# Kernel tuning notes

Hardware: AMD Instinct MI355X
Metric: run time of the kernel (lower is better)

Reference implementation:

```python
import jax, jax.numpy as jnp
import numpy as np

B, N, D, H, K = 16, 256, 64, 64, 2  # batch, nodes, d_in, d_hidden, top_k


def setup_inputs() -> dict:
    key = jax.random.key(0)
    k0, k1, k2 = jax.random.split(key, 3)
    O = jax.random.normal(k0, (B, N, D), dtype=jnp.float32)
    # PairwiseFeaturizer.proj: Linear(4*D, H) -> ReLU -> Linear(H, 1)
    W1 = jax.random.normal(k1, (4 * D, H), dtype=jnp.float32) / np.sqrt(4 * D).astype(np.float32)
    b1 = jnp.zeros((H,), dtype=jnp.float32)
    W2 = jax.random.normal(k2, (H, 1), dtype=jnp.float32) / np.sqrt(H).astype(np.float32)
    b2 = jnp.zeros((1,), dtype=jnp.float32)
    return {"O": O, "W1": W1, "b1": b1, "W2": W2, "b2": b2}


def reference(O, W1, b1, W2, b2):
    Bn, Nn, d = O.shape
    ii, jj = jnp.triu_indices(Nn, k=1)  # all undirected pairs i<j, M = N(N-1)/2
    Oi = O[:, ii, :]  # (B, M, d) gather
    Oj = O[:, jj, :]  # (B, M, d) gather
    feats = jnp.concatenate([Oi, Oj, jnp.abs(Oi - Oj), Oi * Oj], axis=-1)  # (B, M, 4d)
    h = jax.nn.relu(jnp.einsum('bmf,fh->bmh', feats, W1) + b1)
    Q = (jnp.einsum('bmh,ho->bmo', h, W2) + b2)[..., 0]  # (B, M)
    # greedy top-k selection mask (eps -> 0 limit of select_pairs)
    idx = jax.lax.top_k(Q, K)[1]  # (B, K)
    mask = jnp.zeros(Q.shape, dtype=bool).at[jnp.arange(Q.shape[0])[:, None], idx].set(True)
    return Q, mask
```

## Files before the change

kernel.cpp:

```cpp
#include <hip/hip_runtime.h>
#include <math.h>

#define Bn 16
#define Nn 256
#define Mm (Nn*(Nn-1)/2)
#define CHUNK 4080

typedef __attribute__((ext_vector_type(8))) short bf16x8;
typedef __attribute__((ext_vector_type(4))) short short4v;
typedef __attribute__((ext_vector_type(4))) float f32x4;

typedef union { bf16x8 v; short s[8]; __bf16 h[8]; } F8;
typedef union { short4v v; __bf16 h[4]; } F4;

#define MFMA(acc, a, b) \
  acc = __builtin_amdgcn_mfma_f32_16x16x32_bf16((a), (b), (acc), 0, 0, 0)

__device__ __forceinline__ void top2_update(float v, int m,
    float& v1, int& i1, float& v2, int& i2)
{
  bool c1 = (v > v1) || (v == v1 && m < i1);
  bool c2 = (v > v2) || (v == v2 && m < i2);
  float nv2 = c1 ? v1 : (c2 ? v : v2);
  int   ni2 = c1 ? i1 : (c2 ? m : i2);
  v1 = c1 ? v : v1;  i1 = c1 ? m : i1;
  v2 = nv2;          i2 = ni2;
}

__global__ __launch_bounds__(256) void prep_w1t(
    const float* __restrict__ W1, unsigned short* __restrict__ wtg)
{
  const int h = blockIdx.x;
  const int k = threadIdx.x;
  __bf16 b = (__bf16)W1[k * 64 + h];
  wtg[h * 256 + k] = *(unsigned short*)&b;
}

__global__ __launch_bounds__(256) void prep_ac(
    const float* __restrict__ O, const float* __restrict__ b1,
    const unsigned short* __restrict__ wtg,
    unsigned short* __restrict__ obg, float* __restrict__ Ag,
    unsigned short* __restrict__ Cgb)
{
  __shared__ __align__(16) unsigned short s_ob[64][72];
  const int t = threadIdx.x, l = t & 63, wv = t >> 6;
  const int lo = l & 15, g = l >> 4;
  const int b = blockIdx.x >> 2, rt = blockIdx.x & 3;
  const int r0 = rt * 64;
  const float* Ob = O + ((size_t)b * Nn + r0) * 64;

  #pragma unroll
  for (int p = 0; p < 4; ++p) {
    int v = t + p * 256;
    int r = v >> 4, c4 = (v & 15) * 4;
    float4 x = ((const float4*)Ob)[v];
    F4 pk; pk.h[0] = (__bf16)x.x; pk.h[1] = (__bf16)x.y;
           pk.h[2] = (__bf16)x.z; pk.h[3] = (__bf16)x.w;
    *(short4v*)&s_ob[r][c4] = pk.v;
    *(short4v*)&obg[((size_t)b * Nn + r0 + r) * 64 + c4] = pk.v;
  }
  __syncthreads();

  F8 aop[2];
  #pragma unroll
  for (int ks = 0; ks < 2; ++ks)
    aop[ks].v = *(const bf16x8*)&s_ob[wv * 16 + lo][ks * 32 + g * 8];

  #pragma unroll
  for (int half = 0; half < 2; ++half) {
    #pragma unroll
    for (int nf = 0; nf < 4; ++nf) {
      f32x4 ac = {0.f, 0.f, 0.f, 0.f};
      #pragma unroll
      for (int ks = 0; ks < 2; ++ks) {
        F8 bop; bop.v = *(const bf16x8*)&wtg[(nf * 16 + lo) * 256 + half * 64 + ks * 32 + g * 8];
        MFMA(ac, aop[ks].v, bop.v);
      }
      const int h = nf * 16 + lo;
      if (half == 0) {
        float bb = b1[h];
        #pragma unroll
        for (int r = 0; r < 4; ++r)
          Ag[((size_t)b * Nn + r0 + wv * 16 + g * 4 + r) * 64 + h] = ac[r] + bb;
      } else {
        #pragma unroll
        for (int r = 0; r < 4; ++r) {
          __bf16 cb = (__bf16)ac[r];
          Cgb[((size_t)b * Nn + r0 + wv * 16 + g * 4 + r) * 64 + h] = *(unsigned short*)&cb;
        }
      }
    }
  }
}

__global__ __launch_bounds__(256, 2) void pair_kernel(
    const unsigned short* __restrict__ obg,
    const float* __restrict__ Ag,
    const unsigned short* __restrict__ Cgb,
    const float* __restrict__ W2,
    const float* __restrict__ b2,
    const unsigned short* __restrict__ wtg,
    float* __restrict__ Q,
    float* __restrict__ cand)
{
  __shared__ __align__(16) unsigned short s_wt[64][136];
  __shared__ float s_w2[64];
  __shared__ float s_red[4][4];

  const int t  = threadIdx.x;
  const int l  = t & 63, wv = t >> 6;
  const int lo = l & 15, g = l >> 4;

  const int blk    = blockIdx.x;
  const int within = blk >> 3;
  const int batch  = (blk & 7) * 2 + within / 72;
  int tl           = within % 72;
  int a = 0;
  while (tl >= 8 - (a >> 1)) { tl -= 8 - (a >> 1); ++a; }
  const int c   = (a >> 1) + tl;
  const int ti0 = a * 16, tj0 = c * 32;
  const bool diag = (tj0 == ti0 * 2 && (a & 1) == 0) ? false : false;
  const bool dg = (c * 32 < ti0 + 16) || (c == 0 && a == 0) ? false : false; (void)dg;
  const bool isdiag = (tj0 < ti0 + 16);

  const size_t obase = (size_t)batch * Nn;
  const size_t qbase = (size_t)batch * Mm;

  {
    const int h = t >> 2, kq = (t & 3) * 32;
    #pragma unroll
    for (int q = 0; q < 4; ++q)
      *(bf16x8*)&s_wt[h][kq + q * 8] =
          *(const bf16x8*)&wtg[h * 256 + 128 + kq + q * 8];
    if (t < 64) s_w2[t] = W2[t];
  }
  __syncthreads();

  F8 bfr[4][4];
  #pragma unroll
  for (int ks = 0; ks < 4; ++ks)
    #pragma unroll
    for (int nf = 0; nf < 4; ++nf)
      bfr[ks][nf].v = *(const bf16x8*)&s_wt[nf * 16 + lo][ks * 32 + g * 8];

  F8 ojb[2][2];
  #pragma unroll
  for (int jh = 0; jh < 2; ++jh) {
    ojb[jh][0].v = *(const bf16x8*)&obg[(obase + tj0 + jh * 16 + lo) * 64 + g * 8];
    ojb[jh][1].v = *(const bf16x8*)&obg[(obase + tj0 + jh * 16 + lo) * 64 + 32 + g * 8];
  }
  F4 cinb[2][4];
  #pragma unroll
  for (int jh = 0; jh < 2; ++jh)
    #pragma unroll
    for (int nf = 0; nf < 4; ++nf)
      cinb[jh][nf].v = *(const short4v*)
          &Cgb[(obase + tj0 + jh * 16 + lo) * 64 + nf * 16 + g * 4];

  const float b2v = b2[0];

  F8 oib0, oib1;
  f32x4 as4[4];
  int iG = 0, mbG = 0;
  int iP = 0, mbP = 0;
  f32x4 acc0[4], acc1[4];
  F8 f0, f1, f2, f3;
  float v1 = -INFINITY, v2 = -INFINITY;
  int   i1 = 0x7fffffff, i2 = 0x7fffffff;

  auto LOADROW = [&](int ii) {
    const int i = ti0 + wv * 4 + ii;
    oib0.v = *(const bf16x8*)&obg[(obase + i) * 64 + g * 8];
    oib1.v = *(const bf16x8*)&obg[(obase + i) * 64 + 32 + g * 8];
    #pragma unroll
    for (int nf = 0; nf < 4; ++nf)
      as4[nf] = *(const f32x4*)&Ag[(obase + i) * 64 + nf * 16 + g * 4];
    iG = i;
    mbG = i * (Nn - 1) - (i * (i - 1)) / 2 - i - 1;
  };

  auto BUILD = [&](const F8& oj0, const F8& oj1) {
    #pragma unroll
    for (int e = 0; e < 8; ++e) {
      float oi0 = (float)oib0.h[e], oi1 = (float)oib1.h[e];
      float p0  = (float)oj0.h[e],  p1  = (float)oj1.h[e];
      f0.h[e] = (__bf16)fabsf(oi0 - p0);
      f1.h[e] = (__bf16)fabsf(oi1 - p1);
      f2.h[e] = (__bf16)(oi0 * p0);
      f3.h[e] = (__bf16)(oi1 * p1);
    }
  };

  auto STEP = [&](f32x4 (&acc)[4]) {
    #pragma unroll
    for (int nf = 0; nf < 4; ++nf) acc[nf] = as4[nf];
    MFMA(acc[0], bfr[0][0].v, f0.v); MFMA(acc[1], bfr[0][1].v, f0.v);
    MFMA(acc[2], bfr[0][2].v, f0.v); MFMA(acc[3], bfr[0][3].v, f0.v);
    MFMA(acc[0], bfr[1][0].v, f1.v); MFMA(acc[1], bfr[1][1].v, f1.v);
    MFMA(acc[2], bfr[1][2].v, f1.v); MFMA(acc[3], bfr[1][3].v, f1.v);
    MFMA(acc[0], bfr[2][0].v, f2.v); MFMA(acc[1], bfr[2][1].v, f2.v);
    MFMA(acc[2], bfr[2][2].v, f2.v); MFMA(acc[3], bfr[2][3].v, f2.v);
    MFMA(acc[0], bfr[3][0].v, f3.v); MFMA(acc[1], bfr[3][1].v, f3.v);
    MFMA(acc[2], bfr[3][2].v, f3.v); MFMA(acc[3], bfr[3][3].v, f3.v);
  };

  auto EPI = [&](f32x4 (&acc)[4], int jhE, int iE, int mbE) {
    float part = 0.f;
    #pragma unroll
    for (int nf = 0; nf < 4; ++nf) {
      f32x4 w2v = *(const f32x4*)&s_w2[nf * 16 + g * 4];
      #pragma unroll
      for (int r = 0; r < 4; ++r) {
        float z = acc[nf][r] + (float)cinb[jhE][nf].h[r];
        part = fmaf(fmaxf(z, 0.f), w2v[r], part);
      }
    }
    part += __shfl_xor(part, 16);
    part += __shfl_xor(part, 32);
    if (l < 16) {
      const int j = tj0 + jhE * 16 + l;
      if (!isdiag || j > iE) {
        const float qv = part + b2v;
        const int m = mbE + j;
        Q[qbase + m] = qv;
        top2_update(qv, m, v1, i1, v2, i2);
      }
    }
  };

  LOADROW(0);
  BUILD(ojb[0][0], ojb[0][1]); STEP(acc0);
  BUILD(ojb[1][0], ojb[1][1]); STEP(acc1); EPI(acc0, 0, iG, mbG);

  iP = iG; mbP = mbG; LOADROW(1);
  EPI(acc1, 1, iP, mbP);
  BUILD(ojb[0][0], ojb[0][1]); STEP(acc0);
  BUILD(ojb[1][0], ojb[1][1]); STEP(acc1); EPI(acc0, 0, iG, mbG);

  iP = iG; mbP = mbG; LOADROW(2);
  EPI(acc1, 1, iP, mbP);
  BUILD(ojb[0][0], ojb[0][1]); STEP(acc0);
  BUILD(ojb[1][0], ojb[1][1]); STEP(acc1); EPI(acc0, 0, iG, mbG);

  iP = iG; mbP = mbG; LOADROW(3);
  EPI(acc1, 1, iP, mbP);
  BUILD(ojb[0][0], ojb[0][1]); STEP(acc0);
  BUILD(ojb[1][0], ojb[1][1]); STEP(acc1); EPI(acc0, 0, iG, mbG);
  EPI(acc1, 1, iG, mbG);

  #pragma unroll
  for (int s = 1; s < 64; s <<= 1) {
    float u1 = __shfl_xor(v1, s); int j1 = __shfl_xor(i1, s);
    float u2 = __shfl_xor(v2, s); int j2 = __shfl_xor(i2, s);
    top2_update(u1, j1, v1, i1, v2, i2);
    top2_update(u2, j2, v1, i1, v2, i2);
  }
  if (l == 0) {
    s_red[wv][0] = v1; s_red[wv][1] = __int_as_float(i1);
    s_red[wv][2] = v2; s_red[wv][3] = __int_as_float(i2);
  }
  __syncthreads();
  if (t == 0) {
    float a1 = s_red[0][0]; int x1 = __float_as_int(s_red[0][1]);
    float a2 = s_red[0][2]; int x2 = __float_as_int(s_red[0][3]);
    #pragma unroll
    for (int e = 1; e < 4; ++e) {
      top2_update(s_red[e][0], __float_as_int(s_red[e][1]), a1, x1, a2, x2);
      top2_update(s_red[e][2], __float_as_int(s_red[e][3]), a1, x1, a2, x2);
    }
    float* cp = cand + ((size_t)batch * 72 + within % 72) * 4;
    cp[0] = a1; cp[1] = __int_as_float(x1);
    cp[2] = a2; cp[3] = __int_as_float(x2);
  }
}

__global__ __launch_bounds__(256) void rankmask_kernel(
    const float* __restrict__ O, const float* __restrict__ W1,
    const float* __restrict__ b1, const float* __restrict__ W2,
    const float* __restrict__ cand, float* __restrict__ mask)
{
  const int b   = blockIdx.x >> 3;
  const int cch = blockIdx.x & 7;
  const int t   = threadIdx.x;
  const int wv  = t >> 6, h = t & 63;
  __shared__ float s_cv[144];
  __shared__ int   s_ci[144];
  __shared__ int   s_m[8];
  __shared__ int   s_ij[8][2];
  __shared__ float s_or[8][2][64];
  __shared__ float s_qe[8];
  __shared__ int   s_k0, s_k1;

  if (t < 144) {
    const float* cp = cand + (size_t)(b * 72 + (t >> 1)) * 4;
    s_cv[t] = cp[(t & 1) * 2];
    s_ci[t] = __float_as_int(cp[(t & 1) * 2 + 1]);
  }
  __syncthreads();
  if (t < 144) {
    float v = s_cv[t]; int m = s_ci[t];
    int rank = 0;
    for (int e = 0; e < 144; ++e) {
      float u = s_cv[e]; int n = s_ci[e];
      rank += (u > v || (u == v && n < m)) ? 1 : 0;
    }
    if (rank < 8) s_m[rank] = m;
  }
  __syncthreads();
  if (t < 16) {
    int m = s_m[t >> 1];
    int i = 0, rem = m;
    while (rem >= Nn - 1 - i) { rem -= Nn - 1 - i; ++i; }
    int j = i + 1 + rem;
    s_ij[t >> 1][t & 1] = (t & 1) ? j : i;
  }
  __syncthreads();
  {
    int cc = t >> 5, rr = (t >> 4) & 1, c4 = (t & 15) * 4;
    int row = s_ij[cc][rr];
    *(float4*)&s_or[cc][rr][c4] = *(const float4*)&O[((size_t)b * Nn + row) * 64 + c4];
  }
  __syncthreads();
  #pragma unroll
  for (int p = 0; p < 2; ++p) {
    const int cc = p * 4 + wv;
    float z = b1[h];
    #pragma unroll 8
    for (int d = 0; d < 64; ++d) {
      float oi = s_or[cc][0][d], oj = s_or[cc][1][d];
      float f3 = fabsf(oi - oj), f4 = oi * oj;
      z += oi * W1[d * 64 + h] + oj * W1[(64 + d) * 64 + h]
         + f3 * W1[(128 + d) * 64 + h] + f4 * W1[(192 + d) * 64 + h];
    }
    float part = fmaxf(z, 0.f) * W2[h];
    #pragma unroll
    for (int s = 1; s < 64; s <<= 1) part += __shfl_xor(part, s);
    if (h == 0) s_qe[cc] = part;
  }
  __syncthreads();
  if (t == 0) {
    float v1 = -INFINITY, v2 = -INFINITY;
    int   i1 = 0x7fffffff, i2 = 0x7fffffff;
    for (int e = 0; e < 8; ++e)
      top2_update(s_qe[e], s_m[e], v1, i1, v2, i2);
    s_k0 = i1; s_k1 = i2;
  }
  __syncthreads();

  const int k0 = s_k0, k1 = s_k1;
  float* mb = mask + (size_t)b * Mm;
  const int m0 = cch * CHUNK;
  for (int m = m0 + t; m < m0 + CHUNK; m += 256)
    mb[m] = (m == k0 || m == k1) ? 1.0f : 0.0f;
}

extern "C" void kernel_launch(void* const* d_in, const int* in_sizes, int n_in,
                              void* d_out, int out_size, void* d_ws, size_t ws_size,
                              hipStream_t stream) {
  const float* O  = (const float*)d_in[0];
  const float* W1 = (const float*)d_in[1];
  const float* b1 = (const float*)d_in[2];
  const float* W2 = (const float*)d_in[3];
  const float* b2 = (const float*)d_in[4];

  float* Q    = (float*)d_out;
  float* mask = Q + (size_t)Bn * Mm;

  char* ws = (char*)d_ws;
  unsigned short* wtg = (unsigned short*)ws;
  unsigned short* obg = (unsigned short*)(ws + 32768);
  float*          Ag  = (float*)(ws + 32768 + 524288);
  unsigned short* Cgb = (unsigned short*)(ws + 32768 + 524288 + 1048576);
  float*          cand = (float*)(ws + 32768 + 524288 + 1048576 + 524288);

  prep_w1t<<<dim3(64), dim3(256), 0, stream>>>(W1, wtg);
  prep_ac<<<dim3(Bn * 4), dim3(256), 0, stream>>>(O, b1, wtg, obg, Ag, Cgb);
  pair_kernel<<<dim3(Bn * 72), dim3(256), 0, stream>>>(obg, Ag, Cgb, W2, b2, wtg, Q, cand);
  rankmask_kernel<<<dim3(Bn * 8), dim3(256), 0, stream>>>(O, W1, b1, W2, cand, mask);
}
```

Before: 64.96 us.

## Switch pair features to fp16 packed math and merge prep kernels

```diff
diff --git a/kernel.cpp b/kernel.cpp
--- a/kernel.cpp
+++ b/kernel.cpp
@@ -6,15 +6,15 @@
 #define Mm (Nn*(Nn-1)/2)
 #define CHUNK 4080
 
-typedef __attribute__((ext_vector_type(8))) short bf16x8;
-typedef __attribute__((ext_vector_type(4))) short short4v;
+typedef __attribute__((ext_vector_type(8))) _Float16 f16x8;
+typedef __attribute__((ext_vector_type(4))) _Float16 f16x4;
 typedef __attribute__((ext_vector_type(4))) float f32x4;
 
-typedef union { bf16x8 v; short s[8]; __bf16 h[8]; } F8;
-typedef union { short4v v; __bf16 h[4]; } F4;
+typedef union { f16x8 v; _Float16 h[8]; unsigned u[4]; } H8;
+typedef union { f16x4 v; _Float16 h[4]; } H4;
 
 #define MFMA(acc, a, b) \
-  acc = __builtin_amdgcn_mfma_f32_16x16x32_bf16((a), (b), (acc), 0, 0, 0)
+  acc = __builtin_amdgcn_mfma_f32_16x16x32_f16((a), (b), (acc), 0, 0, 0)
 
 __device__ __forceinline__ void top2_update(float v, int m,
     float& v1, int& i1, float& v2, int& i2)
@@ -27,25 +27,25 @@
   v2 = nv2;          i2 = ni2;
 }
 
-__global__ __launch_bounds__(256) void prep_w1t(
-    const float* __restrict__ W1, unsigned short* __restrict__ wtg)
+__global__ __launch_bounds__(256) void prep_all(
+    const float* __restrict__ O, const float* __restrict__ W1,
+    const float* __restrict__ b1,
+    _Float16* __restrict__ wtg, _Float16* __restrict__ obg,
+    float* __restrict__ Ag, _Float16* __restrict__ Cgh)
 {
-  const int h = blockIdx.x;
-  const int k = threadIdx.x;
-  __bf16 b = (__bf16)W1[k * 64 + h];
-  wtg[h * 256 + k] = *(unsigned short*)&b;
-}
-
-__global__ __launch_bounds__(256) void prep_ac(
-    const float* __restrict__ O, const float* __restrict__ b1,
-    const unsigned short* __restrict__ wtg,
-    unsigned short* __restrict__ obg, float* __restrict__ Ag,
-    unsigned short* __restrict__ Cgb)
-{
-  __shared__ __align__(16) unsigned short s_ob[64][72];
-  const int t = threadIdx.x, l = t & 63, wv = t >> 6;
+  const int t = threadIdx.x;
+  if (blockIdx.x < 64) {
+    const int h = blockIdx.x;
+    wtg[h * 256 + t] = (_Float16)W1[t * 64 + h];
+    return;
+  }
+
+  __shared__ __align__(16) _Float16 s_ob[64][72];
+  __shared__ __align__(16) _Float16 s_w[64][136];
+  const int l = t & 63, wv = t >> 6;
   const int lo = l & 15, g = l >> 4;
-  const int b = blockIdx.x >> 2, rt = blockIdx.x & 3;
+  const int bb = blockIdx.x - 64;
+  const int b = bb >> 2, rt = bb & 3;
   const int r0 = rt * 64;
   const float* Ob = O + ((size_t)b * Nn + r0) * 64;
 
@@ -54,17 +54,22 @@
     int v = t + p * 256;
     int r = v >> 4, c4 = (v & 15) * 4;
     float4 x = ((const float4*)Ob)[v];
-    F4 pk; pk.h[0] = (__bf16)x.x; pk.h[1] = (__bf16)x.y;
-           pk.h[2] = (__bf16)x.z; pk.h[3] = (__bf16)x.w;
-    *(short4v*)&s_ob[r][c4] = pk.v;
-    *(short4v*)&obg[((size_t)b * Nn + r0 + r) * 64 + c4] = pk.v;
-  }
-  __syncthreads();
-
-  F8 aop[2];
+    H4 pk; pk.h[0] = (_Float16)x.x; pk.h[1] = (_Float16)x.y;
+           pk.h[2] = (_Float16)x.z; pk.h[3] = (_Float16)x.w;
+    *(f16x4*)&s_ob[r][c4] = pk.v;
+    *(f16x4*)&obg[((size_t)b * Nn + r0 + r) * 64 + c4] = pk.v;
+  }
+  #pragma unroll
+  for (int p = 0; p < 32; ++p) {
+    int kk = p * 4 + (t >> 6), h = t & 63;
+    s_w[h][kk] = (_Float16)W1[kk * 64 + h];
+  }
+  __syncthreads();
+
+  H8 aop[2];
   #pragma unroll
   for (int ks = 0; ks < 2; ++ks)
-    aop[ks].v = *(const bf16x8*)&s_ob[wv * 16 + lo][ks * 32 + g * 8];
+    aop[ks].v = *(const f16x8*)&s_ob[wv * 16 + lo][ks * 32 + g * 8];
 
   #pragma unroll
   for (int half = 0; half < 2; ++half) {
@@ -73,37 +78,35 @@
       f32x4 ac = {0.f, 0.f, 0.f, 0.f};
       #pragma unroll
       for (int ks = 0; ks < 2; ++ks) {
-        F8 bop; bop.v = *(const bf16x8*)&wtg[(nf * 16 + lo) * 256 + half * 64 + ks * 32 + g * 8];
+        H8 bop; bop.v = *(const f16x8*)&s_w[nf * 16 + lo][half * 64 + ks * 32 + g * 8];
         MFMA(ac, aop[ks].v, bop.v);
       }
       const int h = nf * 16 + lo;
       if (half == 0) {
-        float bb = b1[h];
+        float bbv = b1[h];
         #pragma unroll
         for (int r = 0; r < 4; ++r)
-          Ag[((size_t)b * Nn + r0 + wv * 16 + g * 4 + r) * 64 + h] = ac[r] + bb;
+          Ag[((size_t)b * Nn + r0 + wv * 16 + g * 4 + r) * 64 + h] = ac[r] + bbv;
       } else {
         #pragma unroll
-        for (int r = 0; r < 4; ++r) {
-          __bf16 cb = (__bf16)ac[r];
-          Cgb[((size_t)b * Nn + r0 + wv * 16 + g * 4 + r) * 64 + h] = *(unsigned short*)&cb;
-        }
+        for (int r = 0; r < 4; ++r)
+          Cgh[((size_t)b * Nn + r0 + wv * 16 + g * 4 + r) * 64 + h] = (_Float16)ac[r];
       }
     }
   }
 }
 
 __global__ __launch_bounds__(256, 2) void pair_kernel(
-    const unsigned short* __restrict__ obg,
+    const _Float16* __restrict__ obg,
     const float* __restrict__ Ag,
-    const unsigned short* __restrict__ Cgb,
+    const _Float16* __restrict__ Cgh,
     const float* __restrict__ W2,
     const float* __restrict__ b2,
-    const unsigned short* __restrict__ wtg,
+    const _Float16* __restrict__ wtg,
     float* __restrict__ Q,
     float* __restrict__ cand)
 {
-  __shared__ __align__(16) unsigned short s_wt[64][136];
+  __shared__ __align__(16) _Float16 s_wt[64][136];
   __shared__ float s_w2[64];
   __shared__ float s_red[4][4];
 
@@ -119,8 +122,6 @@
   while (tl >= 8 - (a >> 1)) { tl -= 8 - (a >> 1); ++a; }
   const int c   = (a >> 1) + tl;
   const int ti0 = a * 16, tj0 = c * 32;
-  const bool diag = (tj0 == ti0 * 2 && (a & 1) == 0) ? false : false;
-  const bool dg = (c * 32 < ti0 + 16) || (c == 0 && a == 0) ? false : false; (void)dg;
   const bool isdiag = (tj0 < ti0 + 16);
 
   const size_t obase = (size_t)batch * Nn;
@@ -130,48 +131,50 @@
     const int h = t >> 2, kq = (t & 3) * 32;
     #pragma unroll
     for (int q = 0; q < 4; ++q)
-      *(bf16x8*)&s_wt[h][kq + q * 8] =
-          *(const bf16x8*)&wtg[h * 256 + 128 + kq + q * 8];
+      *(f16x8*)&s_wt[h][kq + q * 8] =
+          *(const f16x8*)&wtg[h * 256 + 128 + kq + q * 8];
     if (t < 64) s_w2[t] = W2[t];
   }
   __syncthreads();
 
-  F8 bfr[4][4];
+  H8 bfr[4][4];
   #pragma unroll
   for (int ks = 0; ks < 4; ++ks)
     #pragma unroll
     for (int nf = 0; nf < 4; ++nf)
-      bfr[ks][nf].v = *(const bf16x8*)&s_wt[nf * 16 + lo][ks * 32 + g * 8];
-
-  F8 ojb[2][2];
+      bfr[ks][nf].v = *(const f16x8*)&s_wt[nf * 16 + lo][ks * 32 + g * 8];
+
+  H8 ojb[2][2];
   #pragma unroll
   for (int jh = 0; jh < 2; ++jh) {
-    ojb[jh][0].v = *(const bf16x8*)&obg[(obase + tj0 + jh * 16 + lo) * 64 + g * 8];
-    ojb[jh][1].v = *(const bf16x8*)&obg[(obase + tj0 + jh * 16 + lo) * 64 + 32 + g * 8];
-  }
-  F4 cinb[2][4];
+    ojb[jh][0].v = *(const f16x8*)&obg[(obase + tj0 + jh * 16 + lo) * 64 + g * 8];
+    ojb[jh][1].v = *(const f16x8*)&obg[(obase + tj0 + jh * 16 + lo) * 64 + 32 + g * 8];
+  }
+  f32x4 cinf[2][4];
   #pragma unroll
   for (int jh = 0; jh < 2; ++jh)
     #pragma unroll
-    for (int nf = 0; nf < 4; ++nf)
-      cinb[jh][nf].v = *(const short4v*)
-          &Cgb[(obase + tj0 + jh * 16 + lo) * 64 + nf * 16 + g * 4];
+    for (int nf = 0; nf < 4; ++nf) {
+      H4 cx; cx.v = *(const f16x4*)
+          &Cgh[(obase + tj0 + jh * 16 + lo) * 64 + nf * 16 + g * 4];
+      #pragma unroll
+      for (int r = 0; r < 4; ++r) cinf[jh][nf][r] = (float)cx.h[r];
+    }
 
   const float b2v = b2[0];
 
-  F8 oib0, oib1;
+  H8 oib0, oib1;
   f32x4 as4[4];
-  int iG = 0, mbG = 0;
-  int iP = 0, mbP = 0;
+  int iG = 0, mbG = 0, iP = 0, mbP = 0;
   f32x4 acc0[4], acc1[4];
-  F8 f0, f1, f2, f3;
+  H8 f0, f1, f2, f3;
   float v1 = -INFINITY, v2 = -INFINITY;
   int   i1 = 0x7fffffff, i2 = 0x7fffffff;
 
   auto LOADROW = [&](int ii) {
     const int i = ti0 + wv * 4 + ii;
-    oib0.v = *(const bf16x8*)&obg[(obase + i) * 64 + g * 8];
-    oib1.v = *(const bf16x8*)&obg[(obase + i) * 64 + 32 + g * 8];
+    oib0.v = *(const f16x8*)&obg[(obase + i) * 64 + g * 8];
+    oib1.v = *(const f16x8*)&obg[(obase + i) * 64 + 32 + g * 8];
     #pragma unroll
     for (int nf = 0; nf < 4; ++nf)
       as4[nf] = *(const f32x4*)&Ag[(obase + i) * 64 + nf * 16 + g * 4];
@@ -179,16 +182,18 @@
     mbG = i * (Nn - 1) - (i * (i - 1)) / 2 - i - 1;
   };
 
-  auto BUILD = [&](const F8& oj0, const F8& oj1) {
-    #pragma unroll
-    for (int e = 0; e < 8; ++e) {
-      float oi0 = (float)oib0.h[e], oi1 = (float)oib1.h[e];
-      float p0  = (float)oj0.h[e],  p1  = (float)oj1.h[e];
-      f0.h[e] = (__bf16)fabsf(oi0 - p0);
-      f1.h[e] = (__bf16)fabsf(oi1 - p1);
-      f2.h[e] = (__bf16)(oi0 * p0);
-      f3.h[e] = (__bf16)(oi1 * p1);
-    }
+  auto BUILD = [&](const H8& oj0, const H8& oj1) {
+    H8 d0, d1;
+    d0.v = oib0.v - oj0.v;
+    d1.v = oib1.v - oj1.v;
+    #pragma unroll
+    for (int q = 0; q < 4; ++q) {
+      d0.u[q] &= 0x7FFF7FFFu;
+      d1.u[q] &= 0x7FFF7FFFu;
+    }
+    f0 = d0; f1 = d1;
+    f2.v = oib0.v * oj0.v;
+    f3.v = oib1.v * oj1.v;
   };
 
   auto STEP = [&](f32x4 (&acc)[4]) {
@@ -211,7 +216,7 @@
       f32x4 w2v = *(const f32x4*)&s_w2[nf * 16 + g * 4];
       #pragma unroll
       for (int r = 0; r < 4; ++r) {
-        float z = acc[nf][r] + (float)cinb[jhE][nf].h[r];
+        float z = acc[nf][r] + cinf[jhE][nf][r];
         part = fmaf(fmaxf(z, 0.f), w2v[r], part);
       }
     }
@@ -367,14 +372,13 @@
   float* mask = Q + (size_t)Bn * Mm;
 
   char* ws = (char*)d_ws;
-  unsigned short* wtg = (unsigned short*)ws;
-  unsigned short* obg = (unsigned short*)(ws + 32768);
-  float*          Ag  = (float*)(ws + 32768 + 524288);
-  unsigned short* Cgb = (unsigned short*)(ws + 32768 + 524288 + 1048576);
-  float*          cand = (float*)(ws + 32768 + 524288 + 1048576 + 524288);
-
-  prep_w1t<<<dim3(64), dim3(256), 0, stream>>>(W1, wtg);
-  prep_ac<<<dim3(Bn * 4), dim3(256), 0, stream>>>(O, b1, wtg, obg, Ag, Cgb);
-  pair_kernel<<<dim3(Bn * 72), dim3(256), 0, stream>>>(obg, Ag, Cgb, W2, b2, wtg, Q, cand);
+  _Float16* wtg = (_Float16*)ws;
+  _Float16* obg = (_Float16*)(ws + 32768);
+  float*    Ag  = (float*)(ws + 32768 + 524288);
+  _Float16* Cgh = (_Float16*)(ws + 32768 + 524288 + 1048576);
+  float*    cand = (float*)(ws + 32768 + 524288 + 1048576 + 524288);
+
+  prep_all<<<dim3(128), dim3(256), 0, stream>>>(O, W1, b1, wtg, obg, Ag, Cgh);
+  pair_kernel<<<dim3(Bn * 72), dim3(256), 0, stream>>>(obg, Ag, Cgh, W2, b2, wtg, Q, cand);
   rankmask_kernel<<<dim3(Bn * 8), dim3(256), 0, stream>>>(O, W1, b1, W2, cand, mask);
 }
```

Result: faster. 58.36 us (-10.1%).
